# Kernel optimization log

Hardware: AMD Instinct MI355X
Metric: run time of the kernel (lower is better)

## Reference

```python
import jax, jax.numpy as jnp
import numpy as np

N, E = 20000, 320000          # nodes, edges
R, B = 9, 9                   # num_relations, num_bases
IN, HID, OUT = 128, 256, 64   # feature dims
EPS = 1e-5                    # LayerNorm eps


def layer_norm(h, gamma, beta):
    mu = jnp.mean(h, axis=-1, keepdims=True)
    var = jnp.var(h, axis=-1, keepdims=True)
    return (h - mu) * jax.lax.rsqrt(var + EPS) * gamma + beta


def rgcn_conv(x, src, dst, etype, bases, comp, root, bias, aggr):
    # basis decomposition: W_r = sum_b comp[r,b] * bases[b]
    W = jnp.einsum('rb,bio->rio', comp, bases)          # [R, in, out]
    xW = jnp.einsum('ni,rio->rno', x, W)                # [R, N, out]
    msg = xW[etype, src]                                # [E, out] gather per edge
    if aggr == 'max':
        agg = jax.ops.segment_max(msg, dst, num_segments=N)
        agg = jnp.where(jnp.isfinite(agg), agg, 0.0)    # empty segments -> 0
    else:
        agg = jax.ops.segment_sum(msg, dst, num_segments=N)
    return agg + x @ root + bias


def setup_inputs() -> dict:
    key = jax.random.key(0)
    ks = jax.random.split(key, 12)
    rn = lambda k, s, sc=0.05: jax.random.normal(k, s, jnp.float32) * sc
    return {
        'x': jax.random.normal(ks[0], (N, IN), jnp.float32),
        'edge_index': jax.random.randint(ks[1], (2, E), 0, N),
        'edge_type': jax.random.randint(ks[2], (E,), 0, R),
        # conv1 params
        'bases1': rn(ks[3], (B, IN, HID)),
        'comp1': rn(ks[4], (R, B), 0.3),
        'root1': rn(ks[5], (IN, HID)),
        'bias1': jnp.zeros((HID,), jnp.float32),
        'g1': jnp.ones((HID,), jnp.float32),
        'b1': jnp.zeros((HID,), jnp.float32),
        # conv2 params
        'bases2': rn(ks[6], (B, HID, OUT)),
        'comp2': rn(ks[7], (R, B), 0.3),
        'root2': rn(ks[8], (HID, OUT)),
        'bias2': jnp.zeros((OUT,), jnp.float32),
        'g2': jnp.ones((OUT,), jnp.float32),
        'b2': jnp.zeros((OUT,), jnp.float32),
    }


def reference(x, edge_index, edge_type, bases1, comp1, root1, bias1, g1, b1,
              bases2, comp2, root2, bias2, g2, b2):
    src, dst = edge_index[0], edge_index[1]
    h = rgcn_conv(x, src, dst, edge_type, bases1, comp1, root1, bias1, 'max')
    h = jax.nn.relu(layer_norm(h, g1, b1))
    # eval mode: edge dropout and feature dropout are identity
    h = rgcn_conv(h, src, dst, edge_type, bases2, comp2, root2, bias2, 'add')
    h = layer_norm(h, g2, b2)
    return jax.nn.log_softmax(h, axis=1)
```

## Files before the change

### kernel.cpp

```cpp
#include <hip/hip_runtime.h>
#include <math.h>

#define NN 20000
#define NE 320000
#define NREL 9
#define NBASES 9
#define D_IN 128
#define D_HID 256
#define D_OUT 64
#define LN_EPS 1e-5f

#define N1 (NREL * D_HID + D_HID)
#define N2 (NREL * D_OUT + D_OUT)
#define NBLK ((NN + 255) / 256)

#define LSTR 40

typedef __attribute__((ext_vector_type(8))) short bf16x8;
typedef __attribute__((ext_vector_type(4))) float f32x4;

__device__ inline ushort f2b(float f) {
    unsigned u = __float_as_uint(f);
    return (ushort)((u + 0x7FFFu + ((u >> 16) & 1u)) >> 16);
}
__device__ inline float b2f(ushort h) { return __uint_as_float(((unsigned)h) << 16); }
__device__ inline unsigned pack2bf(float f0, float f1) {
    return (unsigned)f2b(f0) | ((unsigned)f2b(f1) << 16);
}

__global__ __launch_bounds__(256) void prep_all(
    const float* __restrict__ bases1, const float* __restrict__ comp1, const float* __restrict__ root1,
    const float* __restrict__ bases2, const float* __restrict__ comp2, const float* __restrict__ root2,
    const float* __restrict__ x,
    ushort* __restrict__ w1t, ushort* __restrict__ w2t, ushort* __restrict__ xbf)
{
    const int SZ1 = N1 * D_IN;
    const int SZ2 = N2 * D_HID;
    const int SZX = NN * D_IN;
    int tid = blockIdx.x * 256 + threadIdx.x;
    if (tid < SZ1) {
        int n = tid >> 7, k = tid & 127;
        float s;
        if (n < NREL * D_HID) {
            int r = n >> 8, o = n & 255;
            s = 0.f;
            #pragma unroll
            for (int b = 0; b < NBASES; b++)
                s += comp1[r * NBASES + b] * bases1[(b * D_IN + k) * D_HID + o];
        } else {
            s = root1[k * D_HID + (n - NREL * D_HID)];
        }
        w1t[tid] = f2b(s);
    } else if (tid < SZ1 + SZ2) {
        int j = tid - SZ1;
        int n = j >> 8, k = j & 255;
        float s;
        if (n < NREL * D_OUT) {
            int r = n >> 6, o = n & 63;
            s = 0.f;
            #pragma unroll
            for (int b = 0; b < NBASES; b++)
                s += comp2[r * NBASES + b] * bases2[(b * D_HID + k) * D_OUT + o];
        } else {
            s = root2[k * D_OUT + (n - NREL * D_OUT)];
        }
        w2t[j] = f2b(s);
    } else if (tid < SZ1 + SZ2 + SZX) {
        int j = tid - SZ1 - SZ2;
        xbf[j] = f2b(x[j]);
    }
}

__global__ __launch_bounds__(256) void hist_dst(const int* __restrict__ dst, int* __restrict__ deg)
{
    int e = blockIdx.x * 256 + threadIdx.x;
    if (e < NE) atomicAdd(&deg[dst[e]], 1);
}

__global__ __launch_bounds__(256) void scan_blk(
    const int* __restrict__ deg, int* __restrict__ local, int* __restrict__ bsum)
{
    __shared__ int wsum[4];
    int tid = threadIdx.x, lane = tid & 63, w = tid >> 6;
    int i = blockIdx.x * 256 + tid;
    int v = (i < NN) ? deg[i] : 0;
    int x = v;
    #pragma unroll
    for (int d = 1; d < 64; d <<= 1) {
        int y = __shfl_up(x, d, 64);
        if (lane >= d) x += y;
    }
    if (lane == 63) wsum[w] = x;
    __syncthreads();
    int woff = 0;
    for (int j = 0; j < w; j++) woff += wsum[j];
    if (i < NN) local[i] = woff + x - v;
    if (tid == 255) bsum[blockIdx.x] = woff + x;
}

__global__ __launch_bounds__(64) void scan_top(const int* __restrict__ bsum, int* __restrict__ boff)
{
    int lane = threadIdx.x;
    int carry = 0;
    for (int base = 0; base < NBLK; base += 64) {
        int i = base + lane;
        int v = (i < NBLK) ? bsum[i] : 0;
        int x = v;
        #pragma unroll
        for (int d = 1; d < 64; d <<= 1) {
            int y = __shfl_up(x, d, 64);
            if (lane >= d) x += y;
        }
        if (i < NBLK) boff[i] = carry + x - v;
        carry += __shfl(x, 63, 64);
    }
}

__global__ __launch_bounds__(256) void scan_fin(
    const int* __restrict__ local, const int* __restrict__ boff,
    int* __restrict__ offs, int* __restrict__ cursor)
{
    int i = blockIdx.x * 256 + threadIdx.x;
    if (i < NN) {
        int o = local[i] + boff[i >> 8];
        offs[i] = o;
        cursor[i] = o;
    }
    if (i == NN) offs[NN] = NE;
}

__global__ __launch_bounds__(256) void scatter_ep(
    const int* __restrict__ src, const int* __restrict__ dst, const int* __restrict__ etype,
    int* __restrict__ cursor, int* __restrict__ ep1, int* __restrict__ ep2)
{
    int e = blockIdx.x * 256 + threadIdx.x;
    if (e >= NE) return;
    int d = dst[e];
    int s = src[e], r = etype[e];
    int pos = atomicAdd(&cursor[d], 1);
    ep1[pos] = s * N1 + r * D_HID;
    ep2[pos] = s * N2 + r * D_OUT;
}

__global__ __launch_bounds__(256) void gemm_bf16(
    const ushort* __restrict__ A, const ushort* __restrict__ Bt, ushort* __restrict__ C,
    int M, int N, int K)
{
    __shared__ ushort As[2][128 * LSTR];
    __shared__ ushort Bs[2][128 * LSTR];

    int tid = threadIdx.x;
    int lane = tid & 63, w = tid >> 6;
    int wm = w >> 1, wn = w & 1;
    int row0 = blockIdx.y * 128, col0 = blockIdx.x * 128;

    int r0 = tid >> 2, q0 = tid & 3;
    int arow0 = min(row0 + r0, M - 1);
    int arow1 = min(row0 + r0 + 64, M - 1);
    const ushort* gA0 = &A[(size_t)arow0 * K + q0 * 8];
    const ushort* gA1 = &A[(size_t)arow1 * K + q0 * 8];
    const ushort* gB0 = &Bt[(size_t)(col0 + r0) * K + q0 * 8];
    const ushort* gB1 = &Bt[(size_t)(col0 + r0 + 64) * K + q0 * 8];
    int lo0 = r0 * LSTR + q0 * 8;
    int lo1 = (r0 + 64) * LSTR + q0 * 8;

    f32x4 acc[4][4];
    #pragma unroll
    for (int mt = 0; mt < 4; mt++)
        #pragma unroll
        for (int nt = 0; nt < 4; nt++)
            acc[mt][nt] = (f32x4){0.f, 0.f, 0.f, 0.f};

    {
        bf16x8 a0 = *(const bf16x8*)gA0;
        bf16x8 a1 = *(const bf16x8*)gA1;
        bf16x8 b0 = *(const bf16x8*)gB0;
        bf16x8 b1 = *(const bf16x8*)gB1;
        *(bf16x8*)&As[0][lo0] = a0;
        *(bf16x8*)&As[0][lo1] = a1;
        *(bf16x8*)&Bs[0][lo0] = b0;
        *(bf16x8*)&Bs[0][lo1] = b1;
    }

    int mr = lane & 15, kq = lane >> 4;
    const int NC = K >> 5;
    for (int c = 0; c < NC; c++) {
        __syncthreads();
        int cur = c & 1, nxt = cur ^ 1;
        bf16x8 a0, a1, b0, b1;
        bool more = (c + 1 < NC);
        if (more) {
            gA0 += 32; gA1 += 32; gB0 += 32; gB1 += 32;
            a0 = *(const bf16x8*)gA0;
            a1 = *(const bf16x8*)gA1;
            b0 = *(const bf16x8*)gB0;
            b1 = *(const bf16x8*)gB1;
        }

        bf16x8 af[4], bfr[4];
        #pragma unroll
        for (int mt = 0; mt < 4; mt++)
            af[mt] = *(const bf16x8*)&As[cur][(wm * 64 + mt * 16 + mr) * LSTR + kq * 8];
        #pragma unroll
        for (int nt = 0; nt < 4; nt++)
            bfr[nt] = *(const bf16x8*)&Bs[cur][(wn * 64 + nt * 16 + mr) * LSTR + kq * 8];
        #pragma unroll
        for (int mt = 0; mt < 4; mt++)
            #pragma unroll
            for (int nt = 0; nt < 4; nt++)
                acc[mt][nt] = __builtin_amdgcn_mfma_f32_16x16x32_bf16(
                    bfr[nt], af[mt], acc[mt][nt], 0, 0, 0);

        if (more) {
            *(bf16x8*)&As[nxt][lo0] = a0;
            *(bf16x8*)&As[nxt][lo1] = a1;
            *(bf16x8*)&Bs[nxt][lo0] = b0;
            *(bf16x8*)&Bs[nxt][lo1] = b1;
        }
    }

    int q = lane >> 4, cm = lane & 15;
    #pragma unroll
    for (int mt = 0; mt < 4; mt++) {
        int gr = row0 + wm * 64 + mt * 16 + cm;
        if (gr < M) {
            #pragma unroll
            for (int nt = 0; nt < 4; nt++) {
                int gc = col0 + wn * 64 + nt * 16 + q * 4;
                uint2 o;
                o.x = pack2bf(acc[mt][nt][0], acc[mt][nt][1]);
                o.y = pack2bf(acc[mt][nt][2], acc[mt][nt][3]);
                *(uint2*)&C[(size_t)gr * N + gc] = o;
            }
        }
    }
}

__global__ __launch_bounds__(256) void gather1(
    const ushort* __restrict__ xw1, const int* __restrict__ offs, const int* __restrict__ ep1,
    const float* __restrict__ bias, const float* __restrict__ g, const float* __restrict__ b,
    ushort* __restrict__ h)
{
    int n = blockIdx.x * 4 + (threadIdx.x >> 6);
    if (n >= NN) return;
    int lane = threadIdx.x & 63;
    int lane4 = lane * 4;
    int e0 = __builtin_amdgcn_readfirstlane(offs[n]);
    int e1 = __builtin_amdgcn_readfirstlane(offs[n + 1]);

    float m0 = -INFINITY, m1 = -INFINITY, m2 = -INFINITY, m3 = -INFINITY;
    int e = e0;
    for (; e + 8 <= e1; e += 8) {
        int p[8];
        #pragma unroll
        for (int j = 0; j < 8; j++) p[j] = ep1[e + j];
        ushort4 v[8];
        #pragma unroll
        for (int j = 0; j < 8; j++) v[j] = *(const ushort4*)&xw1[(size_t)(p[j] + lane4)];
        #pragma unroll
        for (int j = 0; j < 8; j++) {
            m0 = fmaxf(m0, b2f(v[j].x)); m1 = fmaxf(m1, b2f(v[j].y));
            m2 = fmaxf(m2, b2f(v[j].z)); m3 = fmaxf(m3, b2f(v[j].w));
        }
    }
    for (; e + 2 <= e1; e += 2) {
        int pa = ep1[e], pb = ep1[e + 1];
        ushort4 va = *(const ushort4*)&xw1[(size_t)(pa + lane4)];
        ushort4 vb = *(const ushort4*)&xw1[(size_t)(pb + lane4)];
        m0 = fmaxf(m0, fmaxf(b2f(va.x), b2f(vb.x)));
        m1 = fmaxf(m1, fmaxf(b2f(va.y), b2f(vb.y)));
        m2 = fmaxf(m2, fmaxf(b2f(va.z), b2f(vb.z)));
        m3 = fmaxf(m3, fmaxf(b2f(va.w), b2f(vb.w)));
    }
    for (; e < e1; e++) {
        int p = ep1[e];
        ushort4 v = *(const ushort4*)&xw1[(size_t)(p + lane4)];
        m0 = fmaxf(m0, b2f(v.x)); m1 = fmaxf(m1, b2f(v.y));
        m2 = fmaxf(m2, b2f(v.z)); m3 = fmaxf(m3, b2f(v.w));
    }
    if (e1 == e0) { m0 = m1 = m2 = m3 = 0.f; }

    ushort4 rt = *(const ushort4*)&xw1[(size_t)n * N1 + NREL * D_HID + lane4];
    int c = lane4;
    float t0 = m0 + b2f(rt.x) + bias[c + 0];
    float t1 = m1 + b2f(rt.y) + bias[c + 1];
    float t2 = m2 + b2f(rt.z) + bias[c + 2];
    float t3 = m3 + b2f(rt.w) + bias[c + 3];

    float s = t0 + t1 + t2 + t3;
    float s2 = t0 * t0 + t1 * t1 + t2 * t2 + t3 * t3;
    #pragma unroll
    for (int m = 32; m >= 1; m >>= 1) {
        s  += __shfl_xor(s,  m, 64);
        s2 += __shfl_xor(s2, m, 64);
    }
    float mu = s * (1.f / D_HID);
    float var = s2 * (1.f / D_HID) - mu * mu;
    float rs = rsqrtf(var + LN_EPS);

    ushort4 o;
    o.x = f2b(fmaxf((t0 - mu) * rs * g[c + 0] + b[c + 0], 0.f));
    o.y = f2b(fmaxf((t1 - mu) * rs * g[c + 1] + b[c + 1], 0.f));
    o.z = f2b(fmaxf((t2 - mu) * rs * g[c + 2] + b[c + 2], 0.f));
    o.w = f2b(fmaxf((t3 - mu) * rs * g[c + 3] + b[c + 3], 0.f));
    *(ushort4*)&h[(size_t)n * D_HID + c] = o;
}

__global__ __launch_bounds__(256) void gather2(
    const ushort* __restrict__ xw2, const int* __restrict__ offs, const int* __restrict__ ep2,
    const float* __restrict__ bias, const float* __restrict__ g, const float* __restrict__ b,
    float* __restrict__ out)
{
    int n = blockIdx.x * 4 + (threadIdx.x >> 6);
    if (n >= NN) return;
    int lane = threadIdx.x & 63;
    int e0 = __builtin_amdgcn_readfirstlane(offs[n]);
    int e1 = __builtin_amdgcn_readfirstlane(offs[n + 1]);

    float s = 0.f;
    int e = e0;
    for (; e + 4 <= e1; e += 4) {
        int p0 = ep2[e + 0], p1 = ep2[e + 1], p2 = ep2[e + 2], p3 = ep2[e + 3];
        float a0 = b2f(xw2[(size_t)(p0 + lane)]);
        float a1 = b2f(xw2[(size_t)(p1 + lane)]);
        float a2 = b2f(xw2[(size_t)(p2 + lane)]);
        float a3 = b2f(xw2[(size_t)(p3 + lane)]);
        s += (a0 + a1) + (a2 + a3);
    }
    for (; e < e1; e++) {
        s += b2f(xw2[(size_t)(ep2[e] + lane)]);
    }
    float v = s + b2f(xw2[(size_t)n * N2 + NREL * D_OUT + lane]) + bias[lane];

    float sm = v, s2 = v * v;
    #pragma unroll
    for (int m = 32; m >= 1; m >>= 1) {
        sm += __shfl_xor(sm, m, 64);
        s2 += __shfl_xor(s2, m, 64);
    }
    float mu = sm * (1.f / D_OUT);
    float var = s2 * (1.f / D_OUT) - mu * mu;
    float y = (v - mu) * rsqrtf(var + LN_EPS) * g[lane] + b[lane];

    float mx = y;
    #pragma unroll
    for (int m = 32; m >= 1; m >>= 1) mx = fmaxf(mx, __shfl_xor(mx, m, 64));
    float ex = __expf(y - mx);
    float se = ex;
    #pragma unroll
    for (int m = 32; m >= 1; m >>= 1) se += __shfl_xor(se, m, 64);
    out[(size_t)n * D_OUT + lane] = y - mx - logf(se);
}

extern "C" void kernel_launch(void* const* d_in, const int* in_sizes, int n_in,
                              void* d_out, int out_size, void* d_ws, size_t ws_size,
                              hipStream_t stream)
{
    const float* x      = (const float*)d_in[0];
    const int*   eidx   = (const int*)  d_in[1];
    const int*   etype  = (const int*)  d_in[2];
    const float* bases1 = (const float*)d_in[3];
    const float* comp1  = (const float*)d_in[4];
    const float* root1  = (const float*)d_in[5];
    const float* bias1  = (const float*)d_in[6];
    const float* g1     = (const float*)d_in[7];
    const float* b1     = (const float*)d_in[8];
    const float* bases2 = (const float*)d_in[9];
    const float* comp2  = (const float*)d_in[10];
    const float* root2  = (const float*)d_in[11];
    const float* bias2  = (const float*)d_in[12];
    const float* g2     = (const float*)d_in[13];
    const float* b2     = (const float*)d_in[14];

    const int* src = eidx;
    const int* dst = eidx + NE;

    char* p = (char*)d_ws;
    auto alloc = [&](size_t bytes) -> char* {
        char* r = p;
        p += (bytes + 255) & ~(size_t)255;
        return r;
    };
    ushort* xbf    = (ushort*)alloc((size_t)NN * D_IN * 2);
    ushort* w1t    = (ushort*)alloc((size_t)N1 * D_IN * 2);
    ushort* w2t    = (ushort*)alloc((size_t)N2 * D_HID * 2);
    ushort* xw1    = (ushort*)alloc((size_t)NN * N1 * 2);
    ushort* xw2    = (ushort*)alloc((size_t)NN * N2 * 2);
    ushort* h      = (ushort*)alloc((size_t)NN * D_HID * 2);
    int*    deg    = (int*)   alloc((size_t)NN * 4);
    int*    local  = (int*)   alloc((size_t)NN * 4);
    int*    bsum   = (int*)   alloc((size_t)NBLK * 4);
    int*    boff   = (int*)   alloc((size_t)NBLK * 4);
    int*    offs   = (int*)   alloc((size_t)(NN + 1) * 4);
    int*    cursor = (int*)   alloc((size_t)NN * 4);
    int*    ep1    = (int*)   alloc((size_t)NE * 4);
    int*    ep2    = (int*)   alloc((size_t)NE * 4);

    const int SZP = N1 * D_IN + N2 * D_HID + NN * D_IN;
    prep_all<<<(SZP + 255) / 256, 256, 0, stream>>>(
        bases1, comp1, root1, bases2, comp2, root2, x, w1t, w2t, xbf);

    hipMemsetAsync(deg, 0, (size_t)NN * 4, stream);
    hist_dst<<<(NE + 255) / 256, 256, 0, stream>>>(dst, deg);
    scan_blk<<<NBLK, 256, 0, stream>>>(deg, local, bsum);
    scan_top<<<1, 64, 0, stream>>>(bsum, boff);
    scan_fin<<<NBLK, 256, 0, stream>>>(local, boff, offs, cursor);
    scatter_ep<<<(NE + 255) / 256, 256, 0, stream>>>(src, dst, etype, cursor, ep1, ep2);

    gemm_bf16<<<dim3(N1 / 128, (NN + 127) / 128), 256, 0, stream>>>(xbf, w1t, xw1, NN, N1, D_IN);
    gather1<<<(NN + 3) / 4, 256, 0, stream>>>(xw1, offs, ep1, bias1, g1, b1, h);

    gemm_bf16<<<dim3(N2 / 128, (NN + 127) / 128), 256, 0, stream>>>(h, w2t, xw2, NN, N2, D_HID);
    gather2<<<(NN + 3) / 4, 256, 0, stream>>>(xw2, offs, ep2, bias2, g2, b2, (float*)d_out);
}
```

Measured before the change: 256.6 us.

## Fuse histogram and scan launches, derive ep2 from ep1, swizzle GEMM LDS

Folds the degree histogram into the prep kernel and the top-level block scan into scan_fin, where every block recomputes it redundantly in shared memory. This removes two kernel launches. The second-layer edge offset array is dropped because it can be recovered from ep1 with a shift, since N1 = 4*N2 and D_HID = 4*D_OUT. The GEMM's padded LDS tiles are replaced by an XOR-style swizzled layout to avoid bank conflicts without padding. The trade-offs are redundant scan work per block and a more intricate indexing scheme.

```diff
diff --git a/kernel.cpp b/kernel.cpp
--- a/kernel.cpp
+++ b/kernel.cpp
@@ -14,8 +14,6 @@
 #define N2 (NREL * D_OUT + D_OUT)
 #define NBLK ((NN + 255) / 256)
 
-#define LSTR 40
-
 typedef __attribute__((ext_vector_type(8))) short bf16x8;
 typedef __attribute__((ext_vector_type(4))) float f32x4;
 
@@ -31,8 +29,9 @@
 __global__ __launch_bounds__(256) void prep_all(
     const float* __restrict__ bases1, const float* __restrict__ comp1, const float* __restrict__ root1,
     const float* __restrict__ bases2, const float* __restrict__ comp2, const float* __restrict__ root2,
-    const float* __restrict__ x,
-    ushort* __restrict__ w1t, ushort* __restrict__ w2t, ushort* __restrict__ xbf)
+    const float* __restrict__ x, const int* __restrict__ dst,
+    ushort* __restrict__ w1t, ushort* __restrict__ w2t, ushort* __restrict__ xbf,
+    int* __restrict__ deg)
 {
     const int SZ1 = N1 * D_IN;
     const int SZ2 = N2 * D_HID;
@@ -68,13 +67,10 @@
     } else if (tid < SZ1 + SZ2 + SZX) {
         int j = tid - SZ1 - SZ2;
         xbf[j] = f2b(x[j]);
-    }
-}
-
-__global__ __launch_bounds__(256) void hist_dst(const int* __restrict__ dst, int* __restrict__ deg)
-{
-    int e = blockIdx.x * 256 + threadIdx.x;
-    if (e < NE) atomicAdd(&deg[dst[e]], 1);
+    } else if (tid < SZ1 + SZ2 + SZX + NE) {
+        int e = tid - SZ1 - SZ2 - SZX;
+        atomicAdd(&deg[dst[e]], 1);
+    }
 }
 
 __global__ __launch_bounds__(256) void scan_blk(
@@ -98,31 +94,31 @@
     if (tid == 255) bsum[blockIdx.x] = woff + x;
 }
 
-__global__ __launch_bounds__(64) void scan_top(const int* __restrict__ bsum, int* __restrict__ boff)
-{
-    int lane = threadIdx.x;
-    int carry = 0;
-    for (int base = 0; base < NBLK; base += 64) {
-        int i = base + lane;
-        int v = (i < NBLK) ? bsum[i] : 0;
-        int x = v;
-        #pragma unroll
-        for (int d = 1; d < 64; d <<= 1) {
-            int y = __shfl_up(x, d, 64);
-            if (lane >= d) x += y;
-        }
-        if (i < NBLK) boff[i] = carry + x - v;
-        carry += __shfl(x, 63, 64);
-    }
-}
-
 __global__ __launch_bounds__(256) void scan_fin(
-    const int* __restrict__ local, const int* __restrict__ boff,
+    const int* __restrict__ local, const int* __restrict__ bsum,
     int* __restrict__ offs, int* __restrict__ cursor)
 {
-    int i = blockIdx.x * 256 + threadIdx.x;
+    __shared__ int boff_s[NBLK];
+    int tid = threadIdx.x;
+    if (tid < 64) {
+        int carry = 0;
+        for (int base = 0; base < NBLK; base += 64) {
+            int i = base + tid;
+            int v = (i < NBLK) ? bsum[i] : 0;
+            int x = v;
+            #pragma unroll
+            for (int d = 1; d < 64; d <<= 1) {
+                int y = __shfl_up(x, d, 64);
+                if (tid >= d) x += y;
+            }
+            if (i < NBLK) boff_s[i] = carry + x - v;
+            carry += __shfl(x, 63, 64);
+        }
+    }
+    __syncthreads();
+    int i = blockIdx.x * 256 + tid;
     if (i < NN) {
-        int o = local[i] + boff[i >> 8];
+        int o = local[i] + boff_s[i >> 8];
         offs[i] = o;
         cursor[i] = o;
     }
@@ -131,7 +127,7 @@
 
 __global__ __launch_bounds__(256) void scatter_ep(
     const int* __restrict__ src, const int* __restrict__ dst, const int* __restrict__ etype,
-    int* __restrict__ cursor, int* __restrict__ ep1, int* __restrict__ ep2)
+    int* __restrict__ cursor, int* __restrict__ ep1)
 {
     int e = blockIdx.x * 256 + threadIdx.x;
     if (e >= NE) return;
@@ -139,15 +135,14 @@
     int s = src[e], r = etype[e];
     int pos = atomicAdd(&cursor[d], 1);
     ep1[pos] = s * N1 + r * D_HID;
-    ep2[pos] = s * N2 + r * D_OUT;
 }
 
 __global__ __launch_bounds__(256) void gemm_bf16(
     const ushort* __restrict__ A, const ushort* __restrict__ Bt, ushort* __restrict__ C,
     int M, int N, int K)
 {
-    __shared__ ushort As[2][128 * LSTR];
-    __shared__ ushort Bs[2][128 * LSTR];
+    __shared__ ushort As[2][512 * 8];
+    __shared__ ushort Bs[2][512 * 8];
 
     int tid = threadIdx.x;
     int lane = tid & 63, w = tid >> 6;
@@ -155,14 +150,19 @@
     int row0 = blockIdx.y * 128, col0 = blockIdx.x * 128;
 
     int r0 = tid >> 2, q0 = tid & 3;
+    int mrw = r0 & 15, gw = r0 >> 4;
+    int sw = q0 * 16 + ((mrw + 2 * q0) & 15);
+    int lo0 = (gw * 64 + sw) * 8;
+    int lo1 = ((gw + 4) * 64 + sw) * 8;
     int arow0 = min(row0 + r0, M - 1);
     int arow1 = min(row0 + r0 + 64, M - 1);
     const ushort* gA0 = &A[(size_t)arow0 * K + q0 * 8];
     const ushort* gA1 = &A[(size_t)arow1 * K + q0 * 8];
     const ushort* gB0 = &Bt[(size_t)(col0 + r0) * K + q0 * 8];
     const ushort* gB1 = &Bt[(size_t)(col0 + r0 + 64) * K + q0 * 8];
-    int lo0 = r0 * LSTR + q0 * 8;
-    int lo1 = (r0 + 64) * LSTR + q0 * 8;
+
+    int mr = lane & 15, kq = lane >> 4;
+    int inner = (kq * 16 + ((mr + 2 * kq) & 15)) * 8;
 
     f32x4 acc[4][4];
     #pragma unroll
@@ -182,7 +182,6 @@
         *(bf16x8*)&Bs[0][lo1] = b1;
     }
 
-    int mr = lane & 15, kq = lane >> 4;
     const int NC = K >> 5;
     for (int c = 0; c < NC; c++) {
         __syncthreads();
@@ -200,10 +199,10 @@
         bf16x8 af[4], bfr[4];
         #pragma unroll
         for (int mt = 0; mt < 4; mt++)
-            af[mt] = *(const bf16x8*)&As[cur][(wm * 64 + mt * 16 + mr) * LSTR + kq * 8];
+            af[mt] = *(const bf16x8*)&As[cur][(size_t)((wm * 4 + mt) * 64) * 8 + inner];
         #pragma unroll
         for (int nt = 0; nt < 4; nt++)
-            bfr[nt] = *(const bf16x8*)&Bs[cur][(wn * 64 + nt * 16 + mr) * LSTR + kq * 8];
+            bfr[nt] = *(const bf16x8*)&Bs[cur][(size_t)((wn * 4 + nt) * 64) * 8 + inner];
         #pragma unroll
         for (int mt = 0; mt < 4; mt++)
             #pragma unroll
@@ -307,7 +306,7 @@
 }
 
 __global__ __launch_bounds__(256) void gather2(
-    const ushort* __restrict__ xw2, const int* __restrict__ offs, const int* __restrict__ ep2,
+    const ushort* __restrict__ xw2, const int* __restrict__ offs, const int* __restrict__ ep1,
     const float* __restrict__ bias, const float* __restrict__ g, const float* __restrict__ b,
     float* __restrict__ out)
 {
@@ -320,7 +319,8 @@
     float s = 0.f;
     int e = e0;
     for (; e + 4 <= e1; e += 4) {
-        int p0 = ep2[e + 0], p1 = ep2[e + 1], p2 = ep2[e + 2], p3 = ep2[e + 3];
+        int p0 = ep1[e + 0] >> 2, p1 = ep1[e + 1] >> 2;
+        int p2 = ep1[e + 2] >> 2, p3 = ep1[e + 3] >> 2;
         float a0 = b2f(xw2[(size_t)(p0 + lane)]);
         float a1 = b2f(xw2[(size_t)(p1 + lane)]);
         float a2 = b2f(xw2[(size_t)(p2 + lane)]);
@@ -328,7 +328,7 @@
         s += (a0 + a1) + (a2 + a3);
     }
     for (; e < e1; e++) {
-        s += b2f(xw2[(size_t)(ep2[e] + lane)]);
+        s += b2f(xw2[(size_t)((ep1[e] >> 2) + lane)]);
     }
     float v = s + b2f(xw2[(size_t)n * N2 + NREL * D_OUT + lane]) + bias[lane];
 
@@ -390,26 +390,22 @@
     int*    deg    = (int*)   alloc((size_t)NN * 4);
     int*    local  = (int*)   alloc((size_t)NN * 4);
     int*    bsum   = (int*)   alloc((size_t)NBLK * 4);
-    int*    boff   = (int*)   alloc((size_t)NBLK * 4);
     int*    offs   = (int*)   alloc((size_t)(NN + 1) * 4);
     int*    cursor = (int*)   alloc((size_t)NN * 4);
     int*    ep1    = (int*)   alloc((size_t)NE * 4);
-    int*    ep2    = (int*)   alloc((size_t)NE * 4);
-
-    const int SZP = N1 * D_IN + N2 * D_HID + NN * D_IN;
+
+    hipMemsetAsync(deg, 0, (size_t)NN * 4, stream);
+    const int SZP = N1 * D_IN + N2 * D_HID + NN * D_IN + NE;
     prep_all<<<(SZP + 255) / 256, 256, 0, stream>>>(
-        bases1, comp1, root1, bases2, comp2, root2, x, w1t, w2t, xbf);
-
-    hipMemsetAsync(deg, 0, (size_t)NN * 4, stream);
-    hist_dst<<<(NE + 255) / 256, 256, 0, stream>>>(dst, deg);
+        bases1, comp1, root1, bases2, comp2, root2, x, dst, w1t, w2t, xbf, deg);
+
     scan_blk<<<NBLK, 256, 0, stream>>>(deg, local, bsum);
-    scan_top<<<1, 64, 0, stream>>>(bsum, boff);
-    scan_fin<<<NBLK, 256, 0, stream>>>(local, boff, offs, cursor);
-    scatter_ep<<<(NE + 255) / 256, 256, 0, stream>>>(src, dst, etype, cursor, ep1, ep2);
+    scan_fin<<<NBLK, 256, 0, stream>>>(local, bsum, offs, cursor);
+    scatter_ep<<<(NE + 255) / 256, 256, 0, stream>>>(src, dst, etype, cursor, ep1);
 
     gemm_bf16<<<dim3(N1 / 128, (NN + 127) / 128), 256, 0, stream>>>(xbf, w1t, xw1, NN, N1, D_IN);
     gather1<<<(NN + 3) / 4, 256, 0, stream>>>(xw1, offs, ep1, bias1, g1, b1, h);
 
     gemm_bf16<<<dim3(N2 / 128, (NN + 127) / 128), 256, 0, stream>>>(h, w2t, xw2, NN, N2, D_HID);
-    gather2<<<(NN + 3) / 4, 256, 0, stream>>>(xw2, offs, ep2, bias2, g2, b2, (float*)d_out);
-}
+    gather2<<<(NN + 3) / 4, 256, 0, stream>>>(xw2, offs, ep1, bias2, g2, b2, (float*)d_out);
+}
```

Result: faster. 251.2 us (-2.1%).
